# Kernel tuning notes

Measured on AMD Instinct MI355X. Metric: run time of the kernel, lower is better.

The kernel has to match this reference:

```python
import jax, jax.numpy as jnp
import numpy as np

D_IN = 128
HID = 32
HEADS = 8
OUT = 16
N = 50000
E = 400000
NEG_SLOPE = 0.2


def setup_inputs() -> dict:
    key = jax.random.key(0)
    ks = jax.random.split(key, 12)
    s = lambda k, sh: jax.random.normal(k, sh, dtype=jnp.float32) * 0.05
    return {
        "x": jax.random.normal(ks[0], (N, D_IN), dtype=jnp.float32),
        "edge_index": jax.random.randint(ks[1], (2, E), 0, N, dtype=jnp.int64),
        # conv_1: GATv2, heads=8, concat=True
        "W1l": s(ks[2], (D_IN, HEADS * HID)),
        "W1r": s(ks[3], (D_IN, HEADS * HID)),
        "att1": s(ks[4], (HEADS, HID)),
        "b1": jnp.zeros((HEADS * HID,), dtype=jnp.float32),
        # conv_2: GATv2, heads=1, concat=False
        "W2l": s(ks[5], (HEADS * HID, HID)),
        "W2r": s(ks[6], (HEADS * HID, HID)),
        "att2": s(ks[7], (1, HID)),
        "b2": jnp.zeros((HID,), dtype=jnp.float32),
        # final linear
        "Wlin": s(ks[8], (HID, OUT)),
        "blin": jnp.zeros((OUT,), dtype=jnp.float32),
    }


def _gatv2(x, src, dst, Wl, Wr, att, bias, n_nodes):
    heads, ch = att.shape
    xl = (x @ Wl).reshape(n_nodes, heads, ch)   # source-side transform
    xr = (x @ Wr).reshape(n_nodes, heads, ch)   # target-side transform
    # per-edge GATv2 score: a^T leaky_relu(xl_i + xr_j)
    e = jax.nn.leaky_relu(xl[src] + xr[dst], NEG_SLOPE)        # [E,H,C]
    logits = jnp.einsum('ehc,hc->eh', e, att)                  # [E,H]
    # segment softmax grouped by destination node
    m = jax.ops.segment_max(logits, dst, num_segments=n_nodes)
    m = jnp.where(jnp.isfinite(m), m, 0.0)
    p = jnp.exp(logits - m[dst])
    denom = jax.ops.segment_sum(p, dst, num_segments=n_nodes)
    alpha = p / jnp.maximum(denom[dst], 1e-16)                 # [E,H]
    # scatter-sum aggregation of weighted source features
    out = jax.ops.segment_sum(alpha[:, :, None] * xl[src], dst, num_segments=n_nodes)
    return out + bias.reshape(1, heads, ch)                    # [N,H,C]


def reference(x, edge_index, W1l, W1r, att1, b1, W2l, W2r, att2, b2, Wlin, blin):
    n = x.shape[0]
    loops = jnp.arange(n, dtype=edge_index.dtype)
    ei = jnp.concatenate([edge_index, jnp.stack([loops, loops])], axis=1)  # add_self_loops=True
    src, dst = ei[0], ei[1]

    h = _gatv2(x, src, dst, W1l, W1r, att1, b1, n)   # [N,8,32]
    h = jax.nn.elu(h.reshape(n, -1))                  # concat=True; dropout=identity (eval)

    h = _gatv2(h, src, dst, W2l, W2r, att2, b2, n)   # [N,1,32]
    h = jax.nn.elu(h[:, 0, :])                        # concat=False, heads=1 -> mean == squeeze

    return h @ Wlin + blin                            # [N,16]
```

## Files before the change

### kernel.cpp

```cpp
#include <hip/hip_runtime.h>
#include <cstdint>
#include <cstddef>

#define N_NODES 50000
#define N_EDGES 400000
#define E_TOT   (N_EDGES + N_NODES)
#define D_INF   128
#define C1      256
#define HIDC    32
#define OUTC    16
#define NEG_SLOPE 0.2f
#define LOG2E   1.44269504088896340736f

#define ESRC_CAP (E_TOT + 3 * N_NODES + 16)

#define TB_W   ((2 * D_INF * C1 + 2 * C1 * HIDC + 255) / 256)
#define DEGB   ((E_TOT + 255) / 256)
#define FILLB  ((E_TOT + 255) / 256)

#define UNITS1 ((N_NODES + 31) / 32)
#define GB1S   ((2 * UNITS1 + 3) / 4)
#define GB2S   ((2 * UNITS1 + 3) / 4)

typedef __bf16 bf16x8 __attribute__((ext_vector_type(8)));
typedef float  floatx4 __attribute__((ext_vector_type(4)));
typedef float  floatx2 __attribute__((ext_vector_type(2)));
typedef unsigned int uintx4 __attribute__((ext_vector_type(4)));
typedef unsigned int uintx2 __attribute__((ext_vector_type(2)));
typedef unsigned short ushortx8 __attribute__((ext_vector_type(8)));
typedef unsigned short ushortx4 __attribute__((ext_vector_type(4)));

__device__ __forceinline__ unsigned short f2bf(float f) {
  unsigned int u = __builtin_bit_cast(unsigned int, f);
  u += 0x7FFFu + ((u >> 16) & 1u);
  return (unsigned short)(u >> 16);
}
__device__ __forceinline__ float bf2f(unsigned short u) {
  return __builtin_bit_cast(float, (unsigned int)u << 16);
}
__device__ __forceinline__ floatx2 bf2x2(unsigned int u) {
  floatx2 r;
  r.x = __builtin_bit_cast(float, u << 16);
  r.y = __builtin_bit_cast(float, u & 0xffff0000u);
  return r;
}

__device__ __forceinline__ int ld_src(const int* ei, int f, int e) {
  return f ? ei[2 * e] : ei[e];
}
__device__ __forceinline__ int ld_dst(const int* ei, int f, int e) {
  return f ? ei[2 * (N_EDGES + e)] : ei[N_EDGES + e];
}

__global__ void k_detect(const int* __restrict__ ei, int* __restrict__ flag) {
  __shared__ int s;
  if (threadIdx.x == 0) s = 0;
  __syncthreads();
  atomicOr(&s, ei[2 * threadIdx.x + 1]);
  __syncthreads();
  if (threadIdx.x == 0) *flag = (s == 0) ? 1 : 0;
}

__global__ __launch_bounds__(256) void k_prep(
    const int* __restrict__ ei, const int* __restrict__ flag,
    const float* __restrict__ W1l, const float* __restrict__ W1r,
    const float* __restrict__ W2l, const float* __restrict__ W2r,
    unsigned short* __restrict__ W1lT, unsigned short* __restrict__ W1rT,
    unsigned short* __restrict__ W2lT, unsigned short* __restrict__ W2rT,
    int* __restrict__ deg) {
  const int bid = blockIdx.x;
  const int tid = threadIdx.x;
  if (bid < DEGB) {
    const int e = bid * 256 + tid;
    if (e < E_TOT) {
      int dst = (e < N_EDGES) ? ld_dst(ei, *flag, e) : (e - N_EDGES);
      if ((unsigned)dst < N_NODES) atomicAdd(&deg[dst], 1);
    }
    return;
  }
  int idx = (bid - DEGB) * 256 + tid;
  if (idx < D_INF * C1) {
    const int r = idx >> 8, c = idx & 255;
    W1lT[c * D_INF + r] = f2bf(W1l[idx]);
  } else if (idx < 2 * D_INF * C1) {
    idx -= D_INF * C1;
    const int r = idx >> 8, c = idx & 255;
    W1rT[c * D_INF + r] = f2bf(W1r[idx]);
  } else if (idx < 2 * D_INF * C1 + C1 * HIDC) {
    idx -= 2 * D_INF * C1;
    const int r = idx >> 5, c = idx & 31;
    W2lT[c * C1 + r] = f2bf(W2l[idx]);
  } else if (idx < 2 * (D_INF * C1 + C1 * HIDC)) {
    idx -= 2 * D_INF * C1 + C1 * HIDC;
    const int r = idx >> 5, c = idx & 31;
    W2rT[c * C1 + r] = f2bf(W2r[idx]);
  }
}

__global__ __launch_bounds__(256) void k_alloc(
    const int* __restrict__ deg, int* __restrict__ rowptr,
    int* __restrict__ cursor, int* __restrict__ total) {
  const int i = blockIdx.x * 256 + threadIdx.x;
  const int lane = threadIdx.x & 63;
  const int d  = (i < N_NODES) ? deg[i] : 0;
  const int d4 = (d + 3) & ~3;
  int incl = d4;
#pragma unroll
  for (int off = 1; off < 64; off <<= 1) {
    int t = __shfl_up(incl, off);
    if (lane >= off) incl += t;
  }
  const int wtot = __shfl(incl, 63);
  int wb = 0;
  if (lane == 63) wb = atomicAdd(total, wtot);
  wb = __shfl(wb, 63);
  if (i < N_NODES) {
    const int e = wb + incl - d4;
    rowptr[i] = e;
    cursor[i] = e;
  }
}

__device__ __forceinline__ bf16x8 load8(const unsigned short* p) {
  uintx4 raw = *reinterpret_cast<const uintx4*>(p);
  return __builtin_bit_cast(bf16x8, raw);
}
__device__ __forceinline__ bf16x8 load8(const float* p) {
  floatx4 a = *reinterpret_cast<const floatx4*>(p);
  floatx4 b = *reinterpret_cast<const floatx4*>(p + 4);
  ushortx8 u;
#pragma unroll
  for (int i = 0; i < 4; ++i) { u[i] = f2bf(a[i]); u[4 + i] = f2bf(b[i]); }
  return __builtin_bit_cast(bf16x8, u);
}

template <int K, int NCOLS, typename AT>
__device__ __forceinline__ void gemm_body(
    int unit, int lane, const AT* __restrict__ A,
    const unsigned short* __restrict__ BT,
    unsigned short* __restrict__ C, int M) {
  const int lo = lane & 15;
  const int q  = lane >> 4;
  const int r0 = unit * 32;
  if (r0 >= M) return;
  const bool two = (r0 + 16) < M;
  constexpr int KB = K / 32;

  bf16x8 afrag[2][KB];
#pragma unroll
  for (int kb = 0; kb < KB; ++kb)
    afrag[0][kb] = load8(A + (size_t)(r0 + lo) * K + kb * 32 + q * 8);
  if (two) {
#pragma unroll
    for (int kb = 0; kb < KB; ++kb)
      afrag[1][kb] = load8(A + (size_t)(r0 + 16 + lo) * K + kb * 32 + q * 8);
  }

#pragma unroll
  for (int nt = 0; nt < NCOLS / 16; ++nt) {
    floatx4 acc0 = {0.f, 0.f, 0.f, 0.f};
    floatx4 acc1 = {0.f, 0.f, 0.f, 0.f};
    const unsigned short* bptr = BT + (size_t)(nt * 16 + lo) * K + q * 8;
#pragma unroll
    for (int kb = 0; kb < KB; ++kb) {
      bf16x8 b = load8(bptr + kb * 32);
      acc0 = __builtin_amdgcn_mfma_f32_16x16x32_bf16(afrag[0][kb], b, acc0, 0, 0, 0);
      if (two)
        acc1 = __builtin_amdgcn_mfma_f32_16x16x32_bf16(afrag[1][kb], b, acc1, 0, 0, 0);
    }
#pragma unroll
    for (int r = 0; r < 4; ++r) {
      C[(size_t)(r0 + q * 4 + r) * NCOLS + nt * 16 + lo] = f2bf(acc0[r]);
      if (two)
        C[(size_t)(r0 + 16 + q * 4 + r) * NCOLS + nt * 16 + lo] = f2bf(acc1[r]);
    }
  }
}

__global__ __launch_bounds__(256) void k_gemm1_fill(
    const float* __restrict__ A,
    const unsigned short* __restrict__ BT0, const unsigned short* __restrict__ BT1,
    unsigned short* __restrict__ C0, unsigned short* __restrict__ C1_,
    const int* __restrict__ ei, const int* __restrict__ flag,
    int* __restrict__ cursor, int* __restrict__ esrc) {
  if (blockIdx.x < GB1S) {
    const int wave = threadIdx.x >> 6;
    const int lane = threadIdx.x & 63;
    const int unit = blockIdx.x * 4 + wave;
    const int o = (unit >= UNITS1) ? 1 : 0;
    const int ru = unit - o * UNITS1;
    gemm_body<D_INF, C1, float>(ru, lane, A, o ? BT1 : BT0, o ? C1_ : C0, N_NODES);
    return;
  }
  const int e = (blockIdx.x - GB1S) * 256 + threadIdx.x;
  if (e < E_TOT) {
    int src, dst;
    if (e < N_EDGES) { src = ld_src(ei, *flag, e); dst = ld_dst(ei, *flag, e); }
    else             { src = dst = e - N_EDGES; }
    if ((unsigned)src < N_NODES && (unsigned)dst < N_NODES) {
      int pos = atomicAdd(&cursor[dst], 1);
      esrc[pos] = src;
    }
  }
}

__global__ __launch_bounds__(256) void k_gemm2(
    const unsigned short* __restrict__ A,
    const unsigned short* __restrict__ BT0, const unsigned short* __restrict__ BT1,
    unsigned short* __restrict__ C0, unsigned short* __restrict__ C1_) {
  const int wave = threadIdx.x >> 6;
  const int lane = threadIdx.x & 63;
  const int unit = blockIdx.x * 4 + wave;
  const int o = (unit >= UNITS1) ? 1 : 0;
  const int ru = unit - o * UNITS1;
  gemm_body<C1, HIDC, unsigned short>(ru, lane, A, o ? BT1 : BT0, o ? C1_ : C0, N_NODES);
}

__global__ __launch_bounds__(256) void k_gat1(
    const unsigned short* __restrict__ xl1, const unsigned short* __restrict__ xr1,
    const float* __restrict__ att1, const float* __restrict__ b1,
    const int* __restrict__ rowptr, const int* __restrict__ deg,
    const int* __restrict__ esrc, unsigned short* __restrict__ h1) {
  const int wave = threadIdx.x >> 6;
  const int lane = threadIdx.x & 63;
  const int dst = blockIdx.x * 4 + wave;
  if (dst >= N_NODES) return;
  const int h = lane >> 5;
  const int w = lane & 31;
  const int cb = w * 8;

  floatx2 xr2v[4], att2v[4];
  {
    uintx4 r = *reinterpret_cast<const uintx4*>(xr1 + (size_t)dst * C1 + cb);
    floatx4 a0 = *reinterpret_cast<const floatx4*>(att1 + cb);
    floatx4 a1 = *reinterpret_cast<const floatx4*>(att1 + cb + 4);
#pragma unroll
    for (int j = 0; j < 4; ++j) xr2v[j] = bf2x2(r[j]);
    att2v[0] = floatx2{a0.x, a0.y} * LOG2E;
    att2v[1] = floatx2{a0.z, a0.w} * LOG2E;
    att2v[2] = floatx2{a1.x, a1.y} * LOG2E;
    att2v[3] = floatx2{a1.z, a1.w} * LOG2E;
  }

  const int beg = rowptr[dst];
  const int n   = deg[dst];
  const int* __restrict__ ep = esrc + beg;

  float l = 0.f;
  floatx2 acc2[4] = {{0.f, 0.f}, {0.f, 0.f}, {0.f, 0.f}, {0.f, 0.f}};

  auto process = [&](uintx4 cur) {
    floatx2 xs2[4];
    floatx2 v2 = {0.f, 0.f};
#pragma unroll
    for (int j = 0; j < 4; ++j) {
      xs2[j] = bf2x2(cur[j]);
      floatx2 s2 = xs2[j] + xr2v[j];
      floatx2 e2 = __builtin_elementwise_max(s2, s2 * NEG_SLOPE);
      v2 = __builtin_elementwise_fma(e2, att2v[j], v2);
    }
    float v = v2.x + v2.y;
    v += __shfl_xor(v, 1);
    v += __shfl_xor(v, 2);
    v = fminf(fmaxf(v, -100.f), 100.f);
    const float p = __builtin_amdgcn_exp2f(v);
    l += p;
    const floatx2 p2 = {p, p};
#pragma unroll
    for (int j = 0; j < 4; ++j)
      acc2[j] = __builtin_elementwise_fma(p2, xs2[j], acc2[j]);
  };

  uintx4 bufa = {0u, 0u, 0u, 0u}, bufb = {0u, 0u, 0u, 0u};
  if (h < n)
    bufa = *reinterpret_cast<const uintx4*>(xl1 + (size_t)ep[h] * C1 + cb);
  if (h + 2 < n)
    bufb = *reinterpret_cast<const uintx4*>(xl1 + (size_t)ep[h + 2] * C1 + cb);
  int i = h;
  while (i < n) {
    process(bufa);
    if (i + 4 < n)
      bufa = *reinterpret_cast<const uintx4*>(xl1 + (size_t)ep[i + 4] * C1 + cb);
    i += 2;
    if (i >= n) break;
    process(bufb);
    if (i + 4 < n)
      bufb = *reinterpret_cast<const uintx4*>(xl1 + (size_t)ep[i + 4] * C1 + cb);
    i += 2;
  }

  l += __shfl_xor(l, 32);
#pragma unroll
  for (int j = 0; j < 4; ++j) {
    acc2[j].x += __shfl_xor(acc2[j].x, 32);
    acc2[j].y += __shfl_xor(acc2[j].y, 32);
  }

  if (h == 0) {
    const float inv = 1.f / fmaxf(l, 1e-16f);
    ushortx8 ob;
#pragma unroll
    for (int j = 0; j < 4; ++j) {
      float z0 = acc2[j].x * inv + b1[cb + 2 * j];
      float z1 = acc2[j].y * inv + b1[cb + 2 * j + 1];
      z0 = z0 > 0.f ? z0 : (__expf(z0) - 1.f);
      z1 = z1 > 0.f ? z1 : (__expf(z1) - 1.f);
      ob[2 * j]     = f2bf(z0);
      ob[2 * j + 1] = f2bf(z1);
    }
    *reinterpret_cast<ushortx8*>(h1 + (size_t)dst * C1 + cb) = ob;
  }
}

__global__ __launch_bounds__(256) void k_gat2(
    const unsigned short* __restrict__ xl2, const unsigned short* __restrict__ xr2,
    const float* __restrict__ att2, const float* __restrict__ b2,
    const float* __restrict__ Wlin, const float* __restrict__ blin,
    const int* __restrict__ rowptr, const int* __restrict__ deg,
    const int* __restrict__ esrc, float* __restrict__ out) {
  __shared__ float sh[4][32];
  const int wave = threadIdx.x >> 6;
  const int lane = threadIdx.x & 63;
  const int dst = blockIdx.x * 4 + wave;
  if (dst >= N_NODES) return;
  const int o8 = lane >> 3;
  const int w = lane & 7;
  const int cb = w * 4;

  floatx2 xr2v[2], att2v[2];
  {
    uintx2 r = *reinterpret_cast<const uintx2*>(xr2 + (size_t)dst * HIDC + cb);
    floatx4 a = *reinterpret_cast<const floatx4*>(att2 + cb);
    xr2v[0] = bf2x2(r[0]);
    xr2v[1] = bf2x2(r[1]);
    att2v[0] = floatx2{a.x, a.y} * LOG2E;
    att2v[1] = floatx2{a.z, a.w} * LOG2E;
  }

  const int beg = rowptr[dst];
  const int n   = deg[dst];
  const int* __restrict__ ep = esrc + beg;

  float l = 0.f;
  floatx2 acc2[2] = {{0.f, 0.f}, {0.f, 0.f}};

  auto process = [&](uintx2 cur) {
    floatx2 xs2[2];
    floatx2 v2 = {0.f, 0.f};
#pragma unroll
    for (int j = 0; j < 2; ++j) {
      xs2[j] = bf2x2(cur[j]);
      floatx2 s2 = xs2[j] + xr2v[j];
      floatx2 e2 = __builtin_elementwise_max(s2, s2 * NEG_SLOPE);
      v2 = __builtin_elementwise_fma(e2, att2v[j], v2);
    }
    float v = v2.x + v2.y;
    v += __shfl_xor(v, 1);
    v += __shfl_xor(v, 2);
    v += __shfl_xor(v, 4);
    v = fminf(fmaxf(v, -100.f), 100.f);
    const float p = __builtin_amdgcn_exp2f(v);
    l += p;
    const floatx2 p2 = {p, p};
#pragma unroll
    for (int j = 0; j < 2; ++j)
      acc2[j] = __builtin_elementwise_fma(p2, xs2[j], acc2[j]);
  };

  uintx2 bufa = {0u, 0u}, bufb = {0u, 0u};
  if (o8 < n)
    bufa = *reinterpret_cast<const uintx2*>(xl2 + (size_t)ep[o8] * HIDC + cb);
  if (o8 + 8 < n)
    bufb = *reinterpret_cast<const uintx2*>(xl2 + (size_t)ep[o8 + 8] * HIDC + cb);
  int i = o8;
  while (i < n) {
    process(bufa);
    if (i + 16 < n)
      bufa = *reinterpret_cast<const uintx2*>(xl2 + (size_t)ep[i + 16] * HIDC + cb);
    i += 8;
    if (i >= n) break;
    process(bufb);
    if (i + 16 < n)
      bufb = *reinterpret_cast<const uintx2*>(xl2 + (size_t)ep[i + 16] * HIDC + cb);
    i += 8;
  }

#pragma unroll
  for (int k = 8; k < 64; k <<= 1) {
    l += __shfl_xor(l, k);
#pragma unroll
    for (int j = 0; j < 2; ++j) {
      acc2[j].x += __shfl_xor(acc2[j].x, k);
      acc2[j].y += __shfl_xor(acc2[j].y, k);
    }
  }

  if (o8 == 0) {
    const float inv = 1.f / fmaxf(l, 1e-16f);
#pragma unroll
    for (int j = 0; j < 2; ++j) {
      float z0 = acc2[j].x * inv + b2[cb + 2 * j];
      float z1 = acc2[j].y * inv + b2[cb + 2 * j + 1];
      z0 = z0 > 0.f ? z0 : (__expf(z0) - 1.f);
      z1 = z1 > 0.f ? z1 : (__expf(z1) - 1.f);
      sh[wave][cb + 2 * j]     = z0;
      sh[wave][cb + 2 * j + 1] = z1;
    }
  }
  if (lane < OUTC) {
    float o = blin[lane];
#pragma unroll
    for (int k = 0; k < 32; ++k)
      o = fmaf(sh[wave][k], Wlin[k * OUTC + lane], o);
    out[(size_t)dst * OUTC + lane] = o;
  }
}

static inline int cdiv(int a, int b) { return (a + b - 1) / b; }

extern "C" void kernel_launch(void* const* d_in, const int* in_sizes, int n_in,
                              void* d_out, int out_size, void* d_ws, size_t ws_size,
                              hipStream_t stream) {
  const float* x    = (const float*)d_in[0];
  const int*   ei   = (const int*)d_in[1];
  const float* W1l  = (const float*)d_in[2];
  const float* W1r  = (const float*)d_in[3];
  const float* att1 = (const float*)d_in[4];
  const float* b1   = (const float*)d_in[5];
  const float* W2l  = (const float*)d_in[6];
  const float* W2r  = (const float*)d_in[7];
  const float* att2 = (const float*)d_in[8];
  const float* b2   = (const float*)d_in[9];
  const float* Wlin = (const float*)d_in[10];
  const float* blin = (const float*)d_in[11];
  float* out = (float*)d_out;

  char* w = (char*)d_ws;
  auto alloc = [&](size_t bytes) -> char* {
    char* p = w;
    w += (bytes + 255) & ~(size_t)255;
    return p;
  };
  char* regionA = alloc((size_t)N_NODES * C1 * 2);
  unsigned short* xl1 = (unsigned short*)regionA;
  unsigned short* xl2 = (unsigned short*)regionA;
  unsigned short* xr2 = (unsigned short*)(regionA + (size_t)N_NODES * HIDC * 2 + 256);
  unsigned short* xr1 = (unsigned short*)alloc((size_t)N_NODES * C1 * 2);
  unsigned short* h1  = xr1;
  unsigned short* W1lT = (unsigned short*)alloc((size_t)D_INF * C1 * 2);
  unsigned short* W1rT = (unsigned short*)alloc((size_t)D_INF * C1 * 2);
  unsigned short* W2lT = (unsigned short*)alloc((size_t)C1 * HIDC * 2);
  unsigned short* W2rT = (unsigned short*)alloc((size_t)C1 * HIDC * 2);
  int* rowptr = (int*)alloc((size_t)N_NODES * 4);
  int* cursor = (int*)alloc((size_t)N_NODES * 4);
  int* deg    = (int*)alloc((size_t)(N_NODES + 1) * 4);
  int* total  = deg + N_NODES;
  int* esrc   = (int*)alloc((size_t)ESRC_CAP * 4);
  int* flag   = (int*)alloc(4);

  hipMemsetAsync(deg, 0, (size_t)(N_NODES + 1) * 4, stream);
  k_detect<<<1, 64, 0, stream>>>(ei, flag);

  k_prep<<<DEGB + TB_W, 256, 0, stream>>>(ei, flag, W1l, W1r, W2l, W2r,
                                          W1lT, W1rT, W2lT, W2rT, deg);

  k_alloc<<<cdiv(N_NODES, 256), 256, 0, stream>>>(deg, rowptr, cursor, total);

  k_gemm1_fill<<<GB1S + FILLB, 256, 0, stream>>>(x, W1lT, W1rT, xl1, xr1,
                                                 ei, flag, cursor, esrc);

  k_gat1<<<cdiv(N_NODES, 4), 256, 0, stream>>>(xl1, xr1, att1, b1,
                                               rowptr, deg, esrc, h1);

  k_gemm2<<<GB2S, 256, 0, stream>>>(h1, W2lT, W2rT, xl2, xr2);

  k_gat2<<<cdiv(N_NODES, 4), 256, 0, stream>>>(xl2, xr2, att2, b2, Wlin, blin,
                                               rowptr, deg, esrc, out);
}
```

Baseline: 270.6 us.

## Pre-convert x to bf16, split GEMM1 from edge fill, use 16-row GEMM units

The prep kernel now also converts x from fp32 to a bf16 buffer, so GEMM1 loads bf16 A fragments instead of converting fp32 in the inner path. The fused GEMM1+fill kernel is split into a standalone GEMM1 launched before k_alloc and a separate fill kernel. Both GEMMs switch from 32-row units to 16-row units per wave, which doubles the wave count but halves B-fragment reuse per wave. This adds an extra 12.8MB write and read pass over x plus one more kernel launch, and drops the overlap between GEMM1 and edge fill.

```diff
diff --git a/kernel.cpp b/kernel.cpp
--- a/kernel.cpp
+++ b/kernel.cpp
@@ -17,10 +17,11 @@
 #define TB_W   ((2 * D_INF * C1 + 2 * C1 * HIDC + 255) / 256)
 #define DEGB   ((E_TOT + 255) / 256)
 #define FILLB  ((E_TOT + 255) / 256)
-
-#define UNITS1 ((N_NODES + 31) / 32)
-#define GB1S   ((2 * UNITS1 + 3) / 4)
-#define GB2S   ((2 * UNITS1 + 3) / 4)
+#define XBB    (N_NODES * D_INF / 8 / 256)
+#define PREPB  (DEGB + XBB + TB_W)
+
+#define UNITS16 (N_NODES / 16)
+#define GB      ((2 * UNITS16 + 3) / 4)
 
 typedef __bf16 bf16x8 __attribute__((ext_vector_type(8)));
 typedef float  floatx4 __attribute__((ext_vector_type(4)));
@@ -63,6 +64,7 @@
 
 __global__ __launch_bounds__(256) void k_prep(
     const int* __restrict__ ei, const int* __restrict__ flag,
+    const float* __restrict__ x, unsigned short* __restrict__ xbf,
     const float* __restrict__ W1l, const float* __restrict__ W1r,
     const float* __restrict__ W2l, const float* __restrict__ W2r,
     unsigned short* __restrict__ W1lT, unsigned short* __restrict__ W1rT,
@@ -78,7 +80,17 @@
     }
     return;
   }
-  int idx = (bid - DEGB) * 256 + tid;
+  if (bid < DEGB + XBB) {
+    const size_t base = ((size_t)(bid - DEGB) * 256 + tid) * 8;
+    floatx4 a = *reinterpret_cast<const floatx4*>(x + base);
+    floatx4 b = *reinterpret_cast<const floatx4*>(x + base + 4);
+    ushortx8 u;
+#pragma unroll
+    for (int i = 0; i < 4; ++i) { u[i] = f2bf(a[i]); u[4 + i] = f2bf(b[i]); }
+    *reinterpret_cast<ushortx8*>(xbf + base) = u;
+    return;
+  }
+  int idx = (bid - DEGB - XBB) * 256 + tid;
   if (idx < D_INF * C1) {
     const int r = idx >> 8, c = idx & 255;
     W1lT[c * D_INF + r] = f2bf(W1l[idx]);
@@ -121,78 +133,9 @@
   }
 }
 
-__device__ __forceinline__ bf16x8 load8(const unsigned short* p) {
-  uintx4 raw = *reinterpret_cast<const uintx4*>(p);
-  return __builtin_bit_cast(bf16x8, raw);
-}
-__device__ __forceinline__ bf16x8 load8(const float* p) {
-  floatx4 a = *reinterpret_cast<const floatx4*>(p);
-  floatx4 b = *reinterpret_cast<const floatx4*>(p + 4);
-  ushortx8 u;
-#pragma unroll
-  for (int i = 0; i < 4; ++i) { u[i] = f2bf(a[i]); u[4 + i] = f2bf(b[i]); }
-  return __builtin_bit_cast(bf16x8, u);
-}
-
-template <int K, int NCOLS, typename AT>
-__device__ __forceinline__ void gemm_body(
-    int unit, int lane, const AT* __restrict__ A,
-    const unsigned short* __restrict__ BT,
-    unsigned short* __restrict__ C, int M) {
-  const int lo = lane & 15;
-  const int q  = lane >> 4;
-  const int r0 = unit * 32;
-  if (r0 >= M) return;
-  const bool two = (r0 + 16) < M;
-  constexpr int KB = K / 32;
-
-  bf16x8 afrag[2][KB];
-#pragma unroll
-  for (int kb = 0; kb < KB; ++kb)
-    afrag[0][kb] = load8(A + (size_t)(r0 + lo) * K + kb * 32 + q * 8);
-  if (two) {
-#pragma unroll
-    for (int kb = 0; kb < KB; ++kb)
-      afrag[1][kb] = load8(A + (size_t)(r0 + 16 + lo) * K + kb * 32 + q * 8);
-  }
-
-#pragma unroll
-  for (int nt = 0; nt < NCOLS / 16; ++nt) {
-    floatx4 acc0 = {0.f, 0.f, 0.f, 0.f};
-    floatx4 acc1 = {0.f, 0.f, 0.f, 0.f};
-    const unsigned short* bptr = BT + (size_t)(nt * 16 + lo) * K + q * 8;
-#pragma unroll
-    for (int kb = 0; kb < KB; ++kb) {
-      bf16x8 b = load8(bptr + kb * 32);
-      acc0 = __builtin_amdgcn_mfma_f32_16x16x32_bf16(afrag[0][kb], b, acc0, 0, 0, 0);
-      if (two)
-        acc1 = __builtin_amdgcn_mfma_f32_16x16x32_bf16(afrag[1][kb], b, acc1, 0, 0, 0);
-    }
-#pragma unroll
-    for (int r = 0; r < 4; ++r) {
-      C[(size_t)(r0 + q * 4 + r) * NCOLS + nt * 16 + lo] = f2bf(acc0[r]);
-      if (two)
-        C[(size_t)(r0 + 16 + q * 4 + r) * NCOLS + nt * 16 + lo] = f2bf(acc1[r]);
-    }
-  }
-}
-
-__global__ __launch_bounds__(256) void k_gemm1_fill(
-    const float* __restrict__ A,
-    const unsigned short* __restrict__ BT0, const unsigned short* __restrict__ BT1,
-    unsigned short* __restrict__ C0, unsigned short* __restrict__ C1_,
-    const int* __restrict__ ei, const int* __restrict__ flag,
-    int* __restrict__ cursor, int* __restrict__ esrc) {
-  if (blockIdx.x < GB1S) {
-    const int wave = threadIdx.x >> 6;
-    const int lane = threadIdx.x & 63;
-    const int unit = blockIdx.x * 4 + wave;
-    const int o = (unit >= UNITS1) ? 1 : 0;
-    const int ru = unit - o * UNITS1;
-    gemm_body<D_INF, C1, float>(ru, lane, A, o ? BT1 : BT0, o ? C1_ : C0, N_NODES);
-    return;
-  }
-  const int e = (blockIdx.x - GB1S) * 256 + threadIdx.x;
+__global__ void k_fill(const int* __restrict__ ei, const int* __restrict__ flag,
+                       int* __restrict__ cursor, int* __restrict__ esrc) {
+  int e = blockIdx.x * 256 + threadIdx.x;
   if (e < E_TOT) {
     int src, dst;
     if (e < N_EDGES) { src = ld_src(ei, *flag, e); dst = ld_dst(ei, *flag, e); }
@@ -204,6 +147,52 @@
   }
 }
 
+__device__ __forceinline__ bf16x8 load8(const unsigned short* p) {
+  uintx4 raw = *reinterpret_cast<const uintx4*>(p);
+  return __builtin_bit_cast(bf16x8, raw);
+}
+
+template <int K, int NCOLS>
+__device__ __forceinline__ void gemm_body16(
+    int unit, int lane, const unsigned short* __restrict__ A,
+    const unsigned short* __restrict__ BT, unsigned short* __restrict__ C) {
+  const int lo = lane & 15;
+  const int q  = lane >> 4;
+  const int r0 = unit * 16;
+  constexpr int KB = K / 32;
+
+  bf16x8 af[KB];
+#pragma unroll
+  for (int kb = 0; kb < KB; ++kb)
+    af[kb] = load8(A + (size_t)(r0 + lo) * K + kb * 32 + q * 8);
+
+#pragma unroll
+  for (int nt = 0; nt < NCOLS / 16; ++nt) {
+    floatx4 acc = {0.f, 0.f, 0.f, 0.f};
+    const unsigned short* bptr = BT + (size_t)(nt * 16 + lo) * K + q * 8;
+#pragma unroll
+    for (int kb = 0; kb < KB; ++kb) {
+      bf16x8 b = load8(bptr + kb * 32);
+      acc = __builtin_amdgcn_mfma_f32_16x16x32_bf16(af[kb], b, acc, 0, 0, 0);
+    }
+#pragma unroll
+    for (int r = 0; r < 4; ++r)
+      C[(size_t)(r0 + q * 4 + r) * NCOLS + nt * 16 + lo] = f2bf(acc[r]);
+  }
+}
+
+__global__ __launch_bounds__(256) void k_gemm1(
+    const unsigned short* __restrict__ A,
+    const unsigned short* __restrict__ BT0, const unsigned short* __restrict__ BT1,
+    unsigned short* __restrict__ C0, unsigned short* __restrict__ C1_) {
+  const int wave = threadIdx.x >> 6;
+  const int lane = threadIdx.x & 63;
+  const int unit = blockIdx.x * 4 + wave;
+  if (unit >= 2 * UNITS16) return;
+  const int o = (unit >= UNITS16) ? 1 : 0;
+  gemm_body16<D_INF, C1>(unit - o * UNITS16, lane, A, o ? BT1 : BT0, o ? C1_ : C0);
+}
+
 __global__ __launch_bounds__(256) void k_gemm2(
     const unsigned short* __restrict__ A,
     const unsigned short* __restrict__ BT0, const unsigned short* __restrict__ BT1,
@@ -211,9 +200,9 @@
   const int wave = threadIdx.x >> 6;
   const int lane = threadIdx.x & 63;
   const int unit = blockIdx.x * 4 + wave;
-  const int o = (unit >= UNITS1) ? 1 : 0;
-  const int ru = unit - o * UNITS1;
-  gemm_body<C1, HIDC, unsigned short>(ru, lane, A, o ? BT1 : BT0, o ? C1_ : C0, N_NODES);
+  if (unit >= 2 * UNITS16) return;
+  const int o = (unit >= UNITS16) ? 1 : 0;
+  gemm_body16<C1, HIDC>(unit - o * UNITS16, lane, A, o ? BT1 : BT0, o ? C1_ : C0);
 }
 
 __global__ __launch_bounds__(256) void k_gat1(
@@ -447,6 +436,7 @@
   unsigned short* xr2 = (unsigned short*)(regionA + (size_t)N_NODES * HIDC * 2 + 256);
   unsigned short* xr1 = (unsigned short*)alloc((size_t)N_NODES * C1 * 2);
   unsigned short* h1  = xr1;
+  unsigned short* xbf  = (unsigned short*)alloc((size_t)N_NODES * D_INF * 2);
   unsigned short* W1lT = (unsigned short*)alloc((size_t)D_INF * C1 * 2);
   unsigned short* W1rT = (unsigned short*)alloc((size_t)D_INF * C1 * 2);
   unsigned short* W2lT = (unsigned short*)alloc((size_t)C1 * HIDC * 2);
@@ -461,18 +451,18 @@
   hipMemsetAsync(deg, 0, (size_t)(N_NODES + 1) * 4, stream);
   k_detect<<<1, 64, 0, stream>>>(ei, flag);
 
-  k_prep<<<DEGB + TB_W, 256, 0, stream>>>(ei, flag, W1l, W1r, W2l, W2r,
-                                          W1lT, W1rT, W2lT, W2rT, deg);
+  k_prep<<<PREPB, 256, 0, stream>>>(ei, flag, x, xbf, W1l, W1r, W2l, W2r,
+                                    W1lT, W1rT, W2lT, W2rT, deg);
+
+  k_gemm1<<<GB, 256, 0, stream>>>(xbf, W1lT, W1rT, xl1, xr1);
 
   k_alloc<<<cdiv(N_NODES, 256), 256, 0, stream>>>(deg, rowptr, cursor, total);
-
-  k_gemm1_fill<<<GB1S + FILLB, 256, 0, stream>>>(x, W1lT, W1rT, xl1, xr1,
-                                                 ei, flag, cursor, esrc);
+  k_fill<<<FILLB, 256, 0, stream>>>(ei, flag, cursor, esrc);
 
   k_gat1<<<cdiv(N_NODES, 4), 256, 0, stream>>>(xl1, xr1, att1, b1,
                                                rowptr, deg, esrc, h1);
 
-  k_gemm2<<<GB2S, 256, 0, stream>>>(h1, W2lT, W2rT, xl2, xr2);
+  k_gemm2<<<GB, 256, 0, stream>>>(h1, W2lT, W2rT, xl2, xr2);
 
   k_gat2<<<cdiv(N_NODES, 4), 256, 0, stream>>>(xl2, xr2, att2, b2, Wlin, blin,
                                                rowptr, deg, esrc, out);
```

New measurement: 301.7 us. 1.11x slower.
